# Performance work log

Hardware: AMD Instinct MI355X
Metric: run time of the kernel (lower is better)

The kernel has to match this reference:

```python
import jax, jax.numpy as jnp
import numpy as np

UNITS = 512
OUT_STEPS = 32
FEAT = 12  # Dense(12) output fed back as LSTM input


def _lstm_cell(x_t, h, c, W, U, b):
    # Keras LSTMCell gate order: i, f, c(bar), o
    z = x_t @ W + h @ U + b                     # [B, 4U]
    i, f, g, o = jnp.split(z, 4, axis=-1)
    i = jax.nn.sigmoid(i)
    f = jax.nn.sigmoid(f)
    g = jnp.tanh(g)
    o = jax.nn.sigmoid(o)
    c_new = f * c + i * g
    h_new = o * jnp.tanh(c_new)
    return h_new, c_new


def setup_inputs() -> dict:
    key = jax.random.key(0)
    ks = jax.random.split(key, 6)
    B, T = 4096, 128
    s_in = 1.0 / np.sqrt(FEAT)
    s_rec = 1.0 / np.sqrt(UNITS)
    return {
        "x":  jax.random.normal(ks[0], (B, T, FEAT), dtype=jnp.float32),
        "W":  jax.random.normal(ks[1], (FEAT, 4 * UNITS), dtype=jnp.float32) * s_in,
        "U":  jax.random.normal(ks[2], (UNITS, 4 * UNITS), dtype=jnp.float32) * s_rec,
        "b":  jnp.zeros((4 * UNITS,), dtype=jnp.float32),
        "Wd": jax.random.normal(ks[4], (UNITS, FEAT), dtype=jnp.float32) * s_rec,
        "bd": jnp.zeros((FEAT,), dtype=jnp.float32),
    }


def reference(x, W, U, b, Wd, bd):
    B = x.shape[0]
    h0 = jnp.zeros((B, UNITS), dtype=x.dtype)
    c0 = jnp.zeros((B, UNITS), dtype=x.dtype)

    # warmup: run LSTM over full input sequence, keep final state
    def warm_step(carry, x_t):
        h, c = carry
        h, c = _lstm_cell(x_t, h, c, W, U, b)
        return (h, c), None

    (h, c), _ = jax.lax.scan(warm_step, (h0, c0), jnp.swapaxes(x, 0, 1))
    pred0 = h @ Wd + bd                          # [B, 12]

    def ar_step(carry, _):
        h, c, pred = carry
        h, c = _lstm_cell(pred, h, c, W, U, b)
        pred = h @ Wd + bd
        return (h, c, pred), pred

    _, preds_rest = jax.lax.scan(ar_step, (h, c, pred0), None, length=OUT_STEPS - 1)
    preds = jnp.concatenate([pred0[None], preds_rest], axis=0)  # [out_steps, B, 12]
    return jnp.transpose(preds, (1, 0, 2))       # [B, out_steps, 12]
```

## Files before the change

kernel.cpp:

```cpp
#include <hip/hip_runtime.h>


typedef __bf16 bf16;
typedef __attribute__((ext_vector_type(8))) __bf16 bf16x8;
typedef __attribute__((ext_vector_type(4))) float f32x4;

#define NB    4096
#define TSEQ  128
#define FEAT  12
#define UNITS 512
#define NZ    2048
#define OUTS  32

#define BM 128
#define BK 64

#define OFF_UT   ((size_t)0)
#define OFF_UTA  (OFF_UT  + (size_t)NZ*UNITS*2)
#define OFF_WT   (OFF_UTA + (size_t)NZ*UNITS*2)
#define OFF_B2   (OFF_WT  + (size_t)NZ*32*2)
#define OFF_WDT  (OFF_B2  + (size_t)NZ*4)
#define OFF_H0   (OFF_WDT + (size_t)16*UNITS*2)
#define OFF_H1   (OFF_H0  + (size_t)NB*UNITS*2)
#define OFF_C    (OFF_H1  + (size_t)NB*UNITS*2)
#define WS_NEED  (OFF_C   + (size_t)NB*UNITS*4)
#define OFF_HALL (WS_NEED)
#define HALL_SL  ((size_t)NB*UNITS)
#define WS_BIG   (OFF_HALL + (size_t)OUTS*NB*UNITS*2)

__device__ __forceinline__ float fast_exp2(float x){ return __builtin_amdgcn_exp2f(x); }
__device__ __forceinline__ float fast_rcp (float x){ return __builtin_amdgcn_rcpf(x); }
__device__ __forceinline__ float sigm_(float x){ return fast_rcp(1.f + fast_exp2(-1.4426950408889634f*x)); }
__device__ __forceinline__ float tanh_(float x){ return 1.f - 2.f*fast_rcp(1.f + fast_exp2(2.8853900817779268f*x)); }

__device__ __forceinline__ size_t bp_off(int n, int k){
  int g  = n >> 9;
  int uc = n & 511;
  int nu = uc >> 5, uo = uc & 31;
  int lnl = uo*4 + g;
  int wn = lnl >> 6, f = (lnl >> 4) & 3, l15 = lnl & 15;
  int it = k >> 6, kk = (k >> 5) & 1, kgrp = (k >> 3) & 3, e = k & 7;
  int frag = (((nu*2 + wn)*4 + f)*8 + it)*2 + kk;
  return (size_t)frag*1024 + kgrp*256 + l15*16 + e*2;
}

__global__ void prep_u_kernel(const float* __restrict__ U, const float* __restrict__ W,
                              const float* __restrict__ Wd,
                              bf16* __restrict__ Utp, bf16* __restrict__ Utap){
  __shared__ float su[64][65];
  __shared__ float sa[64][65];
  const int n0 = blockIdx.x * 64;
  const int k0 = blockIdx.y * 64;
  const int tx = threadIdx.x & 63;
  const int rr = threadIdx.x >> 6;
  #pragma unroll 4
  for (int it = 0; it < 16; ++it){
    int k = it*4 + rr;
    float u = U[(size_t)(k0+k)*NZ + n0 + tx];
    float a = u;
    #pragma unroll
    for (int j = 0; j < FEAT; ++j) a += Wd[(k0+k)*FEAT + j] * W[(size_t)j*NZ + n0 + tx];
    su[tx][k] = u;
    sa[tx][k] = a;
  }
  __syncthreads();
  const int nl = threadIdx.x & 63;
  const int q  = threadIdx.x >> 6;
  const float (*src)[65] = (q & 1) ? sa : su;
  char* dst = (char*)((q & 1) ? Utap : Utp);
  const int kh = (q >> 1) * 32;
  #pragma unroll
  for (int kc = 0; kc < 32; kc += 8){
    bf16x8 v;
    #pragma unroll
    for (int e = 0; e < 8; ++e) v[e] = (bf16)src[nl][kh + kc + e];
    *reinterpret_cast<bf16x8*>(dst + bp_off(n0 + nl, k0 + kh + kc)) = v;
  }
}

__global__ void prep_w_kernel(const float* __restrict__ W, const float* __restrict__ b,
                              const float* __restrict__ bd, const float* __restrict__ Wd,
                              bf16* __restrict__ Wt, float* __restrict__ b2,
                              bf16* __restrict__ Wdt){
  const int n = blockIdx.x*256 + threadIdx.x;
  float acc = b[n];
  #pragma unroll
  for (int j = 0; j < FEAT; ++j){
    float w = W[(size_t)j*NZ + n];
    Wt[(size_t)n*32 + j] = (bf16)w;
    acc += bd[j] * w;
  }
  #pragma unroll
  for (int j = FEAT; j < 32; ++j) Wt[(size_t)n*32 + j] = (bf16)0.f;
  b2[n] = acc;
  if (n < UNITS){
    #pragma unroll
    for (int j = 0; j < FEAT; ++j) Wdt[(size_t)j*UNITS + n] = (bf16)Wd[(size_t)n*FEAT + j];
    #pragma unroll
    for (int j = FEAT; j < 16; ++j) Wdt[(size_t)j*UNITS + n] = (bf16)0.f;
  }
}

template<int HAS_X>
__launch_bounds__(256, 2)
__global__ void lstm_step_kernel(const bf16* __restrict__ hin, bf16* __restrict__ hout,
                                 float* __restrict__ c,
                                 const bf16* __restrict__ Bp,
                                 const float* __restrict__ bias,
                                 const float* __restrict__ xt,
                                 const bf16* __restrict__ Wt)
{
  __shared__ alignas(16) char lds[65536];

  int bid = blockIdx.x;
  bid = (bid & 7) * 64 + (bid >> 3);
  const int mt = bid >> 4;
  const int nu = bid & 15;
  const int m0 = mt * BM;

  const int tid  = threadIdx.x;
  const int lane = tid & 63;
  const int wid  = tid >> 6;
  const int wm   = wid >> 1, wn = wid & 1;
  const int l15  = lane & 15;
  const int kgrp = lane >> 4;
  const int l7   = lane & 7;
  const int l8   = lane >> 3;

  const bf16* agp = hin + (size_t)(m0 + wid*32 + l8)*UNITS + l7*8;
  const int   aoff = (wid*32 + l8)*128 + ((l7 ^ l8) << 4);

  const char* bp = (const char*)Bp + (size_t)(nu*2 + wn)*65536 + kgrp*256 + l15*16;

  f32x4 acc[4][4];
  #pragma unroll
  for (int i = 0; i < 4; ++i)
    #pragma unroll
    for (int j = 0; j < 4; ++j) acc[i][j] = f32x4{0.f,0.f,0.f,0.f};

  bf16x8 rA[2][4];
  bf16x8 rB[2][8];

  auto loadA_set = [&](int s, int k0){
    #pragma unroll
    for (int i = 0; i < 4; ++i)
      rA[s][i] = *reinterpret_cast<const bf16x8*>(agp + (size_t)i*8*UNITS + k0);
  };
  auto loadB_set = [&](int s, int it){
    #pragma unroll
    for (int f = 0; f < 4; ++f)
      #pragma unroll
      for (int kk = 0; kk < 2; ++kk)
        rB[s][f*2+kk] = *reinterpret_cast<const bf16x8*>(bp + f*16384 + it*2048 + kk*1024);
  };
  auto writeA_set = [&](int s, int bi){
    char* A = lds + (bi << 14);
    #pragma unroll
    for (int i = 0; i < 4; ++i)
      *reinterpret_cast<bf16x8*>(A + aoff + i*1024) = rA[s][i];
  };
  auto compute = [&](int bi, int s){
    const char* A = lds + (bi << 14);
    #pragma unroll
    for (int kk = 0; kk < 2; ++kk){
      const int sa = (((kk*4 + kgrp) ^ (l15 & 7)) << 4);
      bf16x8 af[4];
      #pragma unroll
      for (int f = 0; f < 4; ++f)
        af[f] = *reinterpret_cast<const bf16x8*>(A + (wm*64 + f*16 + l15)*128 + sa);
      #pragma unroll
      for (int i = 0; i < 4; ++i)
        #pragma unroll
        for (int j = 0; j < 4; ++j)
          acc[i][j] = __builtin_amdgcn_mfma_f32_16x16x32_bf16(af[i], rB[s][j*2+kk], acc[i][j], 0, 0, 0);
    }
  };

  bf16x8 xa[4], wq[4];
  if (HAS_X){
    #pragma unroll
    for (int f = 0; f < 4; ++f){
      int row = m0 + wm*64 + f*16 + l15;
      const float* xr = xt + (size_t)row * (TSEQ*FEAT);
      bf16x8 v;
      #pragma unroll
      for (int j = 0; j < 8; ++j) v[j] = (bf16)0.f;
      if (kgrp == 0){
        float4 a = *reinterpret_cast<const float4*>(xr);
        float4 b = *reinterpret_cast<const float4*>(xr + 4);
        v[0]=(bf16)a.x; v[1]=(bf16)a.y; v[2]=(bf16)a.z; v[3]=(bf16)a.w;
        v[4]=(bf16)b.x; v[5]=(bf16)b.y; v[6]=(bf16)b.z; v[7]=(bf16)b.w;
      } else if (kgrp == 1){
        float4 a = *reinterpret_cast<const float4*>(xr + 8);
        v[0]=(bf16)a.x; v[1]=(bf16)a.y; v[2]=(bf16)a.z; v[3]=(bf16)a.w;
      }
      xa[f] = v;
      int lnl = wn*64 + f*16 + l15;
      int zc  = ((lnl & 3) << 9) + nu*32 + (lnl >> 2);
      wq[f] = *reinterpret_cast<const bf16x8*>(Wt + (size_t)zc*32 + kgrp*8);
    }
  }
  const int eu  = tid & 31;
  const int erg = tid >> 5;
  const int cu  = nu*32 + eu;
  float bi_ = bias[0*UNITS + cu];
  float bf_ = bias[1*UNITS + cu];
  float bg_ = bias[2*UNITS + cu];
  float bo_ = bias[3*UNITS + cu];

  loadA_set(0, 0);
  loadB_set(0, 0);
  loadA_set(1, BK);
  loadB_set(1, 1);

  const int rbase = m0 + erg*16;
  float cold[16];
  {
    const float* cp = c + (size_t)rbase*UNITS + cu;
    #pragma unroll
    for (int r = 0; r < 16; ++r) cold[r] = cp[(size_t)r*UNITS];
  }

  writeA_set(0, 0);
  asm volatile("s_waitcnt lgkmcnt(0)" ::: "memory");
  __builtin_amdgcn_sched_barrier(0);
  __builtin_amdgcn_s_barrier();

  #pragma unroll
  for (int t = 0; t < 8; ++t){
    const int p = t & 1;
    if (t + 2 < 8) loadA_set(p, (t+2)*BK);
    compute(p, p);
    if (t + 2 < 8) loadB_set(p, t+2);
    if (t < 7){
      writeA_set(p ^ 1, p ^ 1);
      asm volatile("s_waitcnt lgkmcnt(0)" ::: "memory");
      __builtin_amdgcn_sched_barrier(0);
      __builtin_amdgcn_s_barrier();
    }
  }

  if (HAS_X){
    #pragma unroll
    for (int i = 0; i < 4; ++i)
      #pragma unroll
      for (int j = 0; j < 4; ++j)
        acc[i][j] = __builtin_amdgcn_mfma_f32_16x16x32_bf16(xa[i], wq[j], acc[i][j], 0, 0, 0);
  }

  asm volatile("s_waitcnt lgkmcnt(0)" ::: "memory");
  __builtin_amdgcn_sched_barrier(0);
  __builtin_amdgcn_s_barrier();

  #pragma unroll
  for (int fm = 0; fm < 4; ++fm){
    #pragma unroll
    for (int fn = 0; fn < 4; ++fn){
      int col  = wn*64 + fn*16 + l15;
      int srow = wm*16 + fm*4 + kgrp;
      *reinterpret_cast<f32x4*>(lds + col*512 + ((srow ^ (col & 7)) << 4)) = acc[fm][fn];
    }
  }
  asm volatile("s_waitcnt lgkmcnt(0)" ::: "memory");
  __builtin_amdgcn_sched_barrier(0);
  __builtin_amdgcn_s_barrier();

  #pragma unroll
  for (int q = 0; q < 4; ++q){
    const int s = erg*4 + q;
    f32x4 zi = *reinterpret_cast<const f32x4*>(lds + (eu*4+0)*512 + ((s ^ ((eu*4+0)&7)) << 4));
    f32x4 zf = *reinterpret_cast<const f32x4*>(lds + (eu*4+1)*512 + ((s ^ ((eu*4+1)&7)) << 4));
    f32x4 zg = *reinterpret_cast<const f32x4*>(lds + (eu*4+2)*512 + ((s ^ ((eu*4+2)&7)) << 4));
    f32x4 zo = *reinterpret_cast<const f32x4*>(lds + (eu*4+3)*512 + ((s ^ ((eu*4+3)&7)) << 4));
    #pragma unroll
    for (int rr = 0; rr < 4; ++rr){
      int r = q*4 + rr;
      float iv = sigm_(zi[rr] + bi_);
      float fv = sigm_(zf[rr] + bf_);
      float gv = tanh_(zg[rr] + bg_);
      float ov = sigm_(zo[rr] + bo_);
      float cn = fv*cold[r] + iv*gv;
      size_t idx = (size_t)(rbase + r)*UNITS + cu;
      c[idx]    = cn;
      hout[idx] = (bf16)(ov*tanh_(cn));
    }
  }
}

__global__ void pred_all_kernel(const bf16* __restrict__ hbase, size_t slot_stride, int s0,
                                const bf16* __restrict__ Wdt,
                                const float* __restrict__ bd, float* __restrict__ out){
  const int slot = s0 + blockIdx.y;
  const bf16* h  = hbase + (size_t)blockIdx.y * slot_stride;
  const int tid = threadIdx.x, lane = tid & 63, wid = tid >> 6;
  const int l15 = lane & 15, kg = lane >> 4;
  const int r0 = blockIdx.x*64 + wid*16;
  f32x4 acc = f32x4{0.f,0.f,0.f,0.f};
  const bf16* ap = h   + (size_t)(r0 + l15)*UNITS + kg*8;
  const bf16* bp = Wdt + (size_t)l15*UNITS + kg*8;
  #pragma unroll
  for (int ks = 0; ks < 16; ++ks){
    bf16x8 a = *reinterpret_cast<const bf16x8*>(ap + ks*32);
    bf16x8 b = *reinterpret_cast<const bf16x8*>(bp + ks*32);
    acc = __builtin_amdgcn_mfma_f32_16x16x32_bf16(a, b, acc, 0, 0, 0);
  }
  if (l15 < FEAT){
    float bdv = bd[l15];
    #pragma unroll
    for (int r = 0; r < 4; ++r){
      int row = r0 + kg*4 + r;
      out[(size_t)row*(OUTS*FEAT) + slot*FEAT + l15] = acc[r] + bdv;
    }
  }
}

extern "C" void kernel_launch(void* const* d_in, const int* in_sizes, int n_in,
                              void* d_out, int out_size, void* d_ws, size_t ws_size,
                              hipStream_t stream){
  const float* x  = (const float*)d_in[0];
  const float* W  = (const float*)d_in[1];
  const float* U  = (const float*)d_in[2];
  const float* b  = (const float*)d_in[3];
  const float* Wd = (const float*)d_in[4];
  const float* bd = (const float*)d_in[5];
  float* out = (float*)d_out;
  (void)in_sizes; (void)n_in; (void)out_size;
  if (ws_size < WS_NEED) return;
  const bool big = ws_size >= WS_BIG;

  char* ws  = (char*)d_ws;
  bf16* Utp = (bf16*)(ws + OFF_UT);
  bf16* Utap= (bf16*)(ws + OFF_UTA);
  bf16* Wt  = (bf16*)(ws + OFF_WT);
  float* b2 = (float*)(ws + OFF_B2);
  bf16* Wdt = (bf16*)(ws + OFF_WDT);
  bf16* h0  = (bf16*)(ws + OFF_H0);
  bf16* h1  = (bf16*)(ws + OFF_H1);
  float* c  = (float*)(ws + OFF_C);
  bf16* hall= (bf16*)(ws + OFF_HALL);

  hipMemsetAsync(h0, 0, (size_t)NB*UNITS*2, stream);
  hipMemsetAsync(c,  0, (size_t)NB*UNITS*4, stream);
  prep_u_kernel<<<dim3(32, 8), 256, 0, stream>>>(U, W, Wd, Utp, Utap);
  prep_w_kernel<<<8, 256, 0, stream>>>(W, b, bd, Wd, Wt, b2, Wdt);

  if (big){
    bf16* hcur = h0; bf16* hnxt = h1;
    for (int t = 0; t < TSEQ; ++t){
      bf16* dst = (t == TSEQ-1) ? hall : hnxt;
      lstm_step_kernel<1><<<512, 256, 0, stream>>>(hcur, dst, c, Utp, b, x + t*FEAT, Wt);
      hnxt = hcur; hcur = dst;
    }
    for (int s = 1; s < OUTS; ++s)
      lstm_step_kernel<0><<<512, 256, 0, stream>>>(hall + (size_t)(s-1)*HALL_SL,
                                                   hall + (size_t)s*HALL_SL,
                                                   c, Utap, b2, nullptr, nullptr);
    pred_all_kernel<<<dim3(NB/64, OUTS), 256, 0, stream>>>(hall, HALL_SL, 0, Wdt, bd, out);
  } else {
    bf16* hcur = h0; bf16* hnxt = h1;
    for (int t = 0; t < TSEQ; ++t){
      lstm_step_kernel<1><<<512, 256, 0, stream>>>(hcur, hnxt, c, Utp, b, x + t*FEAT, Wt);
      bf16* tmp = hcur; hcur = hnxt; hnxt = tmp;
    }
    pred_all_kernel<<<dim3(NB/64, 1), 256, 0, stream>>>(hcur, 0, 0, Wdt, bd, out);
    for (int s = 1; s < OUTS; ++s){
      lstm_step_kernel<0><<<512, 256, 0, stream>>>(hcur, hnxt, c, Utap, b2, nullptr, nullptr);
      bf16* tmp = hcur; hcur = hnxt; hnxt = tmp;
      pred_all_kernel<<<dim3(NB/64, 1), 256, 0, stream>>>(hcur, 0, s, Wdt, bd, out);
    }
  }
}
```

Before: 3.157 ms.

## Load A operand directly from global into registers, drop LDS staging

The h-state A tile is now loaded straight from global memory into per-wave MFMA operand registers, replacing the shared-memory staging and its per-iteration barriers. Pipelining shrinks from a two-deep to a one-deep register prefetch, and the x/W input loads move into the last iteration. The aim is to remove LDS write/read traffic and block-wide syncs. In exchange, the two waves sharing a row block both fetch the same A data from global/L2, register pressure rises, and there is less latency hiding.

```diff
diff --git a/kernel.cpp b/kernel.cpp
--- a/kernel.cpp
+++ b/kernel.cpp
@@ -124,12 +124,8 @@
   const int wm   = wid >> 1, wn = wid & 1;
   const int l15  = lane & 15;
   const int kgrp = lane >> 4;
-  const int l7   = lane & 7;
-  const int l8   = lane >> 3;
-
-  const bf16* agp = hin + (size_t)(m0 + wid*32 + l8)*UNITS + l7*8;
-  const int   aoff = (wid*32 + l8)*128 + ((l7 ^ l8) << 4);
-
+
+  const bf16* ap = hin + (size_t)(m0 + wm*64 + l15)*UNITS + kgrp*8;
   const char* bp = (const char*)Bp + (size_t)(nu*2 + wn)*65536 + kgrp*256 + l15*16;
 
   f32x4 acc[4][4];
@@ -138,68 +134,27 @@
     #pragma unroll
     for (int j = 0; j < 4; ++j) acc[i][j] = f32x4{0.f,0.f,0.f,0.f};
 
-  bf16x8 rA[2][4];
-  bf16x8 rB[2][8];
-
-  auto loadA_set = [&](int s, int k0){
-    #pragma unroll
-    for (int i = 0; i < 4; ++i)
-      rA[s][i] = *reinterpret_cast<const bf16x8*>(agp + (size_t)i*8*UNITS + k0);
-  };
-  auto loadB_set = [&](int s, int it){
+  bf16x8 rA[2][8], rB[2][8];
+
+  auto loadAB = [&](int s, int it){
     #pragma unroll
     for (int f = 0; f < 4; ++f)
       #pragma unroll
-      for (int kk = 0; kk < 2; ++kk)
+      for (int kk = 0; kk < 2; ++kk){
+        rA[s][f*2+kk] = *reinterpret_cast<const bf16x8*>(ap + f*(16*UNITS) + it*BK + kk*32);
         rB[s][f*2+kk] = *reinterpret_cast<const bf16x8*>(bp + f*16384 + it*2048 + kk*1024);
+      }
   };
-  auto writeA_set = [&](int s, int bi){
-    char* A = lds + (bi << 14);
-    #pragma unroll
-    for (int i = 0; i < 4; ++i)
-      *reinterpret_cast<bf16x8*>(A + aoff + i*1024) = rA[s][i];
-  };
-  auto compute = [&](int bi, int s){
-    const char* A = lds + (bi << 14);
-    #pragma unroll
-    for (int kk = 0; kk < 2; ++kk){
-      const int sa = (((kk*4 + kgrp) ^ (l15 & 7)) << 4);
-      bf16x8 af[4];
-      #pragma unroll
-      for (int f = 0; f < 4; ++f)
-        af[f] = *reinterpret_cast<const bf16x8*>(A + (wm*64 + f*16 + l15)*128 + sa);
+  auto compute = [&](int s){
+    #pragma unroll
+    for (int kk = 0; kk < 2; ++kk)
       #pragma unroll
       for (int i = 0; i < 4; ++i)
         #pragma unroll
         for (int j = 0; j < 4; ++j)
-          acc[i][j] = __builtin_amdgcn_mfma_f32_16x16x32_bf16(af[i], rB[s][j*2+kk], acc[i][j], 0, 0, 0);
-    }
+          acc[i][j] = __builtin_amdgcn_mfma_f32_16x16x32_bf16(rA[s][i*2+kk], rB[s][j*2+kk], acc[i][j], 0, 0, 0);
   };
 
-  bf16x8 xa[4], wq[4];
-  if (HAS_X){
-    #pragma unroll
-    for (int f = 0; f < 4; ++f){
-      int row = m0 + wm*64 + f*16 + l15;
-      const float* xr = xt + (size_t)row * (TSEQ*FEAT);
-      bf16x8 v;
-      #pragma unroll
-      for (int j = 0; j < 8; ++j) v[j] = (bf16)0.f;
-      if (kgrp == 0){
-        float4 a = *reinterpret_cast<const float4*>(xr);
-        float4 b = *reinterpret_cast<const float4*>(xr + 4);
-        v[0]=(bf16)a.x; v[1]=(bf16)a.y; v[2]=(bf16)a.z; v[3]=(bf16)a.w;
-        v[4]=(bf16)b.x; v[5]=(bf16)b.y; v[6]=(bf16)b.z; v[7]=(bf16)b.w;
-      } else if (kgrp == 1){
-        float4 a = *reinterpret_cast<const float4*>(xr + 8);
-        v[0]=(bf16)a.x; v[1]=(bf16)a.y; v[2]=(bf16)a.z; v[3]=(bf16)a.w;
-      }
-      xa[f] = v;
-      int lnl = wn*64 + f*16 + l15;
-      int zc  = ((lnl & 3) << 9) + nu*32 + (lnl >> 2);
-      wq[f] = *reinterpret_cast<const bf16x8*>(Wt + (size_t)zc*32 + kgrp*8);
-    }
-  }
   const int eu  = tid & 31;
   const int erg = tid >> 5;
   const int cu  = nu*32 + eu;
@@ -208,11 +163,7 @@
   float bg_ = bias[2*UNITS + cu];
   float bo_ = bias[3*UNITS + cu];
 
-  loadA_set(0, 0);
-  loadB_set(0, 0);
-  loadA_set(1, BK);
-  loadB_set(1, 1);
-
+  loadAB(0, 0);
   const int rbase = m0 + erg*16;
   float cold[16];
   {
@@ -221,23 +172,35 @@
     for (int r = 0; r < 16; ++r) cold[r] = cp[(size_t)r*UNITS];
   }
 
-  writeA_set(0, 0);
-  asm volatile("s_waitcnt lgkmcnt(0)" ::: "memory");
-  __builtin_amdgcn_sched_barrier(0);
-  __builtin_amdgcn_s_barrier();
-
+  bf16x8 xa[4], wq[4];
   #pragma unroll
   for (int t = 0; t < 8; ++t){
     const int p = t & 1;
-    if (t + 2 < 8) loadA_set(p, (t+2)*BK);
-    compute(p, p);
-    if (t + 2 < 8) loadB_set(p, t+2);
-    if (t < 7){
-      writeA_set(p ^ 1, p ^ 1);
-      asm volatile("s_waitcnt lgkmcnt(0)" ::: "memory");
-      __builtin_amdgcn_sched_barrier(0);
-      __builtin_amdgcn_s_barrier();
-    }
+    if (t < 7) loadAB(p ^ 1, t + 1);
+    if (HAS_X && t == 7){
+      #pragma unroll
+      for (int f = 0; f < 4; ++f){
+        int row = m0 + wm*64 + f*16 + l15;
+        const float* xr = xt + (size_t)row * (TSEQ*FEAT);
+        bf16x8 v;
+        #pragma unroll
+        for (int j = 0; j < 8; ++j) v[j] = (bf16)0.f;
+        if (kgrp == 0){
+          float4 a = *reinterpret_cast<const float4*>(xr);
+          float4 b = *reinterpret_cast<const float4*>(xr + 4);
+          v[0]=(bf16)a.x; v[1]=(bf16)a.y; v[2]=(bf16)a.z; v[3]=(bf16)a.w;
+          v[4]=(bf16)b.x; v[5]=(bf16)b.y; v[6]=(bf16)b.z; v[7]=(bf16)b.w;
+        } else if (kgrp == 1){
+          float4 a = *reinterpret_cast<const float4*>(xr + 8);
+          v[0]=(bf16)a.x; v[1]=(bf16)a.y; v[2]=(bf16)a.z; v[3]=(bf16)a.w;
+        }
+        xa[f] = v;
+        int lnl = wn*64 + f*16 + l15;
+        int zc  = ((lnl & 3) << 9) + nu*32 + (lnl >> 2);
+        wq[f] = *reinterpret_cast<const bf16x8*>(Wt + (size_t)zc*32 + kgrp*8);
+      }
+    }
+    compute(p);
   }
 
   if (HAS_X){
@@ -247,10 +210,6 @@
       for (int j = 0; j < 4; ++j)
         acc[i][j] = __builtin_amdgcn_mfma_f32_16x16x32_bf16(xa[i], wq[j], acc[i][j], 0, 0, 0);
   }
-
-  asm volatile("s_waitcnt lgkmcnt(0)" ::: "memory");
-  __builtin_amdgcn_sched_barrier(0);
-  __builtin_amdgcn_s_barrier();
 
   #pragma unroll
   for (int fm = 0; fm < 4; ++fm){
```

Measured after the change: 4.345 ms. 1.38x slower.
